# Kernel tuning notes

Hardware: AMD Instinct MI355X
Metric: run time of the kernel (lower is better)

## Reference

```python
import jax, jax.numpy as jnp
import numpy as np

MIN_DISTANCE = 1e-07  # min_distance from __init__
N_LEAVES = 16384
WEIGHTS_DIM = 512


def setup_inputs() -> dict:
    key = jax.random.key(0)
    k1, k2, k3 = jax.random.split(key, 3)
    n_nodes = 2 * N_LEAVES - 1  # complete binary tree, heap layout
    x = jax.random.normal(k1, (N_LEAVES, WEIGHTS_DIM), dtype=jnp.float32)
    # per-node AdditionLayer weights (the learnable delta added to parent weights)
    deltas = jax.random.normal(k2, (n_nodes, WEIGHTS_DIM), dtype=jnp.float32) * 0.05
    # per-node heights (increasing toward leaves in expectation; max() guards negatives)
    heights = jax.random.uniform(k3, (n_nodes,), dtype=jnp.float32)
    return {"x": x, "deltas": deltas, "heights": heights}


def reference(x, deltas, heights):
    n_nodes = deltas.shape[0]
    depth = int(np.log2(n_nodes + 1)) - 1  # static
    parent = (np.arange(n_nodes) - 1) // 2  # static heap parents

    # Cumulative weights down the tree, level by level (depth ~14 static iterations).
    # w[node] = sum of deltas along root->node path == curr_weights at that node.
    w_level = deltas[0:1]  # root: zero_vector + delta_root
    for l in range(1, depth + 1):
        start = 2 ** l - 1
        # each parent feeds its two children (left, right) contiguously in heap order
        w_level = jnp.repeat(w_level, 2, axis=0) + deltas[start:start + 2 ** l]
    w_leaves = w_level  # [n_leaves, weights_dim], leaves in left-to-right order

    # Regularizer: curr_weights - input_weights == delta at every node.
    sq = jnp.sum(deltas * deltas, axis=1)  # [n_nodes]
    branch = jnp.maximum(heights[1:] - heights[parent[1:]], MIN_DISTANCE)
    delta_total = sq[0] + jnp.sum(sq[1:] / branch)  # root term undivided (parent is None)

    # Leaf prediction: x[i] @ curr_weights_leaf_i (the 1xN matvec), concatenated over leaves.
    result = jnp.sum(x * w_leaves, axis=1)  # [n_leaves]
    return result, delta_total.reshape(1)
```

## Files before the change

kernel.cpp:

```cpp
#include <hip/hip_runtime.h>


constexpr int   N_LEAVES = 16384;
constexpr int   N_NODES  = 2 * N_LEAVES - 1;
constexpr int   DIM      = 512;
constexpr float MIN_DIST = 1e-7f;
constexpr int   N_UPPER  = 2047;

__device__ __forceinline__ float4 f4add(float4 a, float4 b) {
    return make_float4(a.x + b.x, a.y + b.y, a.z + b.z, a.w + b.w);
}
__device__ __forceinline__ float f4dot(float4 a, float4 b) {
    return a.x * b.x + a.y * b.y + a.z * b.z + a.w * b.w;
}
__device__ __forceinline__ float f4sq(float4 a) { return f4dot(a, a); }

__global__ void zero_scalar_kernel(float* __restrict__ out) {
    if (threadIdx.x == 0) out[N_LEAVES] = 0.0f;
}

__global__ __launch_bounds__(256) void fused_kernel(
        const float* __restrict__ x,
        const float* __restrict__ deltas,
        const float* __restrict__ heights,
        float* __restrict__ out) {
    __shared__ __align__(16) float wtop[DIM];
    __shared__ float sqred[4];

    const int tid  = threadIdx.x;
    const int lane = tid & 63;
    const int wave = tid >> 6;
    const int b    = blockIdx.x;

    float sq_acc = 0.0f;

    if (wave < 2) {
        const int n = 2 * b + wave;
        if (n < N_UPPER) {
            const float4* row = (const float4*)(deltas + (size_t)n * DIM);
            float4 a = row[lane];
            float4 c = row[lane + 64];
            float scale = 1.0f;
            if (n > 0) {
                float br = heights[n] - heights[(n - 1) >> 1];
                scale = 1.0f / fmaxf(br, MIN_DIST);
            }
            sq_acc += (f4sq(a) + f4sq(c)) * scale;
        }
    }

    {
        float2 acc = make_float2(0.0f, 0.0f);
        #pragma unroll
        for (int l = 0; l <= 10; ++l) {
            const int node = ((1 << l) - 1) + (b >> (10 - l));
            const float2* row = (const float2*)(deltas + (size_t)node * DIM);
            float2 v = row[tid];
            acc.x += v.x; acc.y += v.y;
        }
        wtop[2 * tid]     = acc.x;
        wtop[2 * tid + 1] = acc.y;
    }
    __syncthreads();

    const float4 t0 = ((const float4*)wtop)[lane];
    const float4 t1 = ((const float4*)wtop)[lane + 64];

    #pragma unroll
    for (int k = 0; k < 4; ++k) {
        const int leaf = b * 16 + wave * 4 + k;
        const int n14 = (N_LEAVES - 1) + leaf;
        const int n13 = (n14 - 1) >> 1;
        const int n12 = (n13 - 1) >> 1;
        const int n11 = (n12 - 1) >> 1;

        const float4* r14 = (const float4*)(deltas + (size_t)n14 * DIM);
        const float4* r13 = (const float4*)(deltas + (size_t)n13 * DIM);
        const float4* r12 = (const float4*)(deltas + (size_t)n12 * DIM);
        const float4* r11 = (const float4*)(deltas + (size_t)n11 * DIM);
        const float4* xr  = (const float4*)(x      + (size_t)leaf * DIM);

        float4 a14 = r14[lane], c14 = r14[lane + 64];
        float4 a13 = r13[lane], c13 = r13[lane + 64];
        float4 a12 = r12[lane], c12 = r12[lane + 64];
        float4 a11 = r11[lane], c11 = r11[lane + 64];
        float4 xa  = xr[lane],  xc  = xr[lane + 64];

        float4 w0 = f4add(f4add(t0, a14), f4add(a13, f4add(a12, a11)));
        float4 w1 = f4add(f4add(t1, c14), f4add(c13, f4add(c12, c11)));

        float dot = f4dot(xa, w0) + f4dot(xc, w1);
        #pragma unroll
        for (int off = 32; off; off >>= 1) dot += __shfl_xor(dot, off, 64);
        if (lane == 0) out[leaf] = dot;

        {
            float br = heights[n14] - heights[n13];
            sq_acc += (f4sq(a14) + f4sq(c14)) / fmaxf(br, MIN_DIST);
        }
        if ((leaf & 1) == 0) {
            float br = heights[n13] - heights[n12];
            sq_acc += (f4sq(a13) + f4sq(c13)) / fmaxf(br, MIN_DIST);
        }
        if ((leaf & 3) == 0) {
            float br = heights[n12] - heights[n11];
            sq_acc += (f4sq(a12) + f4sq(c12)) / fmaxf(br, MIN_DIST);
        }
        if ((leaf & 7) == 0) {
            const int n10 = (n11 - 1) >> 1;
            float br = heights[n11] - heights[n10];
            sq_acc += (f4sq(a11) + f4sq(c11)) / fmaxf(br, MIN_DIST);
        }
    }

    #pragma unroll
    for (int off = 32; off; off >>= 1) sq_acc += __shfl_xor(sq_acc, off, 64);
    if (lane == 0) sqred[wave] = sq_acc;
    __syncthreads();
    if (tid == 0)
        atomicAdd(out + N_LEAVES, sqred[0] + sqred[1] + sqred[2] + sqred[3]);
}

extern "C" void kernel_launch(void* const* d_in, const int* in_sizes, int n_in,
                              void* d_out, int out_size, void* d_ws, size_t ws_size,
                              hipStream_t stream) {
    const float* x       = (const float*)d_in[0];
    const float* deltas  = (const float*)d_in[1];
    const float* heights = (const float*)d_in[2];
    float* out = (float*)d_out;

    zero_scalar_kernel<<<1, 64, 0, stream>>>(out);
    fused_kernel<<<N_LEAVES / 16, 256, 0, stream>>>(x, deltas, heights, out);
}
```

Measured before the change: 125.6 us.

## Assign one leaf per wave with 4096 blocks and deeper shared prefix

Each block now handles 4 leaves (one per wave) instead of 16, so the grid grows from 1024 to 4096 blocks. The block-shared prefix sum extends to tree levels 0-12, leaving only levels 13 and 14 to be loaded per leaf. Upper-tree regularizer rows (nodes 0-8190) are spread across waves 1 and 2 of every block. Streaming leaf deltas and x rows use nontemporal loads. More parallelism and fewer per-leaf loads are traded for 13 shared-row loads per block, repeated across four times as many blocks and mostly hitting cache, plus four times as many atomics.

Result: slower. 161.1 us (+28.3%).

```diff
diff --git a/kernel.cpp b/kernel.cpp
--- a/kernel.cpp
+++ b/kernel.cpp
@@ -2,18 +2,19 @@
 
 
 constexpr int   N_LEAVES = 16384;
-constexpr int   N_NODES  = 2 * N_LEAVES - 1;
 constexpr int   DIM      = 512;
 constexpr float MIN_DIST = 1e-7f;
-constexpr int   N_UPPER  = 2047;
 
-__device__ __forceinline__ float4 f4add(float4 a, float4 b) {
-    return make_float4(a.x + b.x, a.y + b.y, a.z + b.z, a.w + b.w);
-}
-__device__ __forceinline__ float f4dot(float4 a, float4 b) {
+typedef float v4f __attribute__((ext_vector_type(4)));
+typedef float v2f __attribute__((ext_vector_type(2)));
+
+__device__ __forceinline__ float v4dot(v4f a, v4f b) {
     return a.x * b.x + a.y * b.y + a.z * b.z + a.w * b.w;
 }
-__device__ __forceinline__ float f4sq(float4 a) { return f4dot(a, a); }
+__device__ __forceinline__ float v4sq(v4f a) { return v4dot(a, a); }
+__device__ __forceinline__ v4f ntload(const v4f* p) {
+    return __builtin_nontemporal_load(p);
+}
 
 __global__ void zero_scalar_kernel(float* __restrict__ out) {
     if (threadIdx.x == 0) out[N_LEAVES] = 0.0f;
@@ -34,84 +35,72 @@
 
     float sq_acc = 0.0f;
 
-    if (wave < 2) {
-        const int n = 2 * b + wave;
-        if (n < N_UPPER) {
-            const float4* row = (const float4*)(deltas + (size_t)n * DIM);
-            float4 a = row[lane];
-            float4 c = row[lane + 64];
-            float scale = 1.0f;
-            if (n > 0) {
-                float br = heights[n] - heights[(n - 1) >> 1];
-                scale = 1.0f / fmaxf(br, MIN_DIST);
-            }
-            sq_acc += (f4sq(a) + f4sq(c)) * scale;
-        }
-    }
+    const int leaf = 4 * b + wave;
+    const int n14  = (N_LEAVES - 1) + leaf;
+    const int n13  = (n14 - 1) >> 1;
+    const int n12  = (n13 - 1) >> 1;
+
+    const v4f* r14 = (const v4f*)(deltas + (size_t)n14 * DIM);
+    const v4f* r13 = (const v4f*)(deltas + (size_t)n13 * DIM);
+    const v4f* xr  = (const v4f*)(x      + (size_t)leaf * DIM);
+
+    v4f a14 = ntload(r14 + lane), c14 = ntload(r14 + lane + 64);
+    v4f a13 = r13[lane],          c13 = r13[lane + 64];
+    v4f xa  = ntload(xr + lane),  xc  = ntload(xr + lane + 64);
 
     {
-        float2 acc = make_float2(0.0f, 0.0f);
+        v2f acc = {0.0f, 0.0f};
         #pragma unroll
-        for (int l = 0; l <= 10; ++l) {
-            const int node = ((1 << l) - 1) + (b >> (10 - l));
-            const float2* row = (const float2*)(deltas + (size_t)node * DIM);
-            float2 v = row[tid];
-            acc.x += v.x; acc.y += v.y;
+        for (int l = 0; l <= 12; ++l) {
+            const int node = ((1 << l) - 1) + (b >> (12 - l));
+            const v2f* row = (const v2f*)(deltas + (size_t)node * DIM);
+            v2f v = row[tid];
+            acc += v;
         }
         wtop[2 * tid]     = acc.x;
         wtop[2 * tid + 1] = acc.y;
     }
+
+    if (wave == 1 && b < 4095) {
+        const int n = b;
+        const v4f* row = (const v4f*)(deltas + (size_t)n * DIM);
+        v4f a = row[lane];
+        v4f c = row[lane + 64];
+        float scale = 1.0f;
+        if (n > 0) {
+            float br = heights[n] - heights[(n - 1) >> 1];
+            scale = 1.0f / fmaxf(br, MIN_DIST);
+        }
+        sq_acc += (v4sq(a) + v4sq(c)) * scale;
+    }
+    if (wave == 2) {
+        const int n = 4095 + b;
+        const v4f* row = (const v4f*)(deltas + (size_t)n * DIM);
+        v4f a = row[lane];
+        v4f c = row[lane + 64];
+        float br = heights[n] - heights[(n - 1) >> 1];
+        sq_acc += (v4sq(a) + v4sq(c)) / fmaxf(br, MIN_DIST);
+    }
+
+    {
+        float br = heights[n14] - heights[n13];
+        sq_acc += (v4sq(a14) + v4sq(c14)) / fmaxf(br, MIN_DIST);
+    }
+    if ((leaf & 1) == 0) {
+        float br = heights[n13] - heights[n12];
+        sq_acc += (v4sq(a13) + v4sq(c13)) / fmaxf(br, MIN_DIST);
+    }
+
     __syncthreads();
 
-    const float4 t0 = ((const float4*)wtop)[lane];
-    const float4 t1 = ((const float4*)wtop)[lane + 64];
-
+    const v4f t0 = ((const v4f*)wtop)[lane];
+    const v4f t1 = ((const v4f*)wtop)[lane + 64];
+    v4f w0 = t0 + a13 + a14;
+    v4f w1 = t1 + c13 + c14;
+    float dot = v4dot(xa, w0) + v4dot(xc, w1);
     #pragma unroll
-    for (int k = 0; k < 4; ++k) {
-        const int leaf = b * 16 + wave * 4 + k;
-        const int n14 = (N_LEAVES - 1) + leaf;
-        const int n13 = (n14 - 1) >> 1;
-        const int n12 = (n13 - 1) >> 1;
-        const int n11 = (n12 - 1) >> 1;
-
-        const float4* r14 = (const float4*)(deltas + (size_t)n14 * DIM);
-        const float4* r13 = (const float4*)(deltas + (size_t)n13 * DIM);
-        const float4* r12 = (const float4*)(deltas + (size_t)n12 * DIM);
-        const float4* r11 = (const float4*)(deltas + (size_t)n11 * DIM);
-        const float4* xr  = (const float4*)(x      + (size_t)leaf * DIM);
-
-        float4 a14 = r14[lane], c14 = r14[lane + 64];
-        float4 a13 = r13[lane], c13 = r13[lane + 64];
-        float4 a12 = r12[lane], c12 = r12[lane + 64];
-        float4 a11 = r11[lane], c11 = r11[lane + 64];
-        float4 xa  = xr[lane],  xc  = xr[lane + 64];
-
-        float4 w0 = f4add(f4add(t0, a14), f4add(a13, f4add(a12, a11)));
-        float4 w1 = f4add(f4add(t1, c14), f4add(c13, f4add(c12, c11)));
-
-        float dot = f4dot(xa, w0) + f4dot(xc, w1);
-        #pragma unroll
-        for (int off = 32; off; off >>= 1) dot += __shfl_xor(dot, off, 64);
-        if (lane == 0) out[leaf] = dot;
-
-        {
-            float br = heights[n14] - heights[n13];
-            sq_acc += (f4sq(a14) + f4sq(c14)) / fmaxf(br, MIN_DIST);
-        }
-        if ((leaf & 1) == 0) {
-            float br = heights[n13] - heights[n12];
-            sq_acc += (f4sq(a13) + f4sq(c13)) / fmaxf(br, MIN_DIST);
-        }
-        if ((leaf & 3) == 0) {
-            float br = heights[n12] - heights[n11];
-            sq_acc += (f4sq(a12) + f4sq(c12)) / fmaxf(br, MIN_DIST);
-        }
-        if ((leaf & 7) == 0) {
-            const int n10 = (n11 - 1) >> 1;
-            float br = heights[n11] - heights[n10];
-            sq_acc += (f4sq(a11) + f4sq(c11)) / fmaxf(br, MIN_DIST);
-        }
-    }
+    for (int off = 32; off; off >>= 1) dot += __shfl_xor(dot, off, 64);
+    if (lane == 0) out[leaf] = dot;
 
     #pragma unroll
     for (int off = 32; off; off >>= 1) sq_acc += __shfl_xor(sq_acc, off, 64);
@@ -130,5 +119,5 @@
     float* out = (float*)d_out;
 
     zero_scalar_kernel<<<1, 64, 0, stream>>>(out);
-    fused_kernel<<<N_LEAVES / 16, 256, 0, stream>>>(x, deltas, heights, out);
+    fused_kernel<<<N_LEAVES / 4, 256, 0, stream>>>(x, deltas, heights, out);
 }
```
